# Optimization experiments

Measured on AMD Instinct MI355X. Metric: run time of the kernel, lower is better.

The kernel has to match this reference:

```python
import jax, jax.numpy as jnp
import numpy as np

EPS = 1e-7

def _sample_project(feat, pid, w1, b1, w2, b2):
    # feat: [B, C, H, W]; pid: [P] flat spatial indices into H*W
    B, C, H, W = feat.shape
    fr = jnp.transpose(feat, (0, 2, 3, 1)).reshape(B, H * W, C)  # [B, HW, C]
    x = fr[:, pid, :].reshape(B * pid.shape[0], C)               # gather -> [B*P, C]
    x = jnp.maximum(x @ w1 + b1, 0.0) @ w2 + b2                  # 2-layer MLP
    norm = jnp.sqrt(jnp.sum(x * x, axis=1, keepdims=True))       # L2 over channels
    return x / (norm + EPS)


def setup_inputs() -> dict:
    key = jax.random.key(0)
    ks = jax.random.split(key, 16)
    NC = 256
    shapes = [(16, 256, 128, 128), (16, 512, 64, 64), (16, 1024, 32, 32)]
    inp = {}
    for i, s in enumerate(shapes):
        inp[f"feat{i}"] = jax.random.normal(ks[i], s, dtype=jnp.float32)
        hw = s[2] * s[3]
        inp[f"patch_id{i}"] = jax.random.randint(ks[3 + i], (256,), 0, hw, dtype=jnp.int64)
        C = s[1]
        g = 0.02  # init_gain (normal init)
        inp[f"w1_{i}"] = g * jax.random.normal(ks[6 + 3 * i], (C, NC), dtype=jnp.float32)
        inp[f"b1_{i}"] = jnp.zeros((NC,), dtype=jnp.float32)
        inp[f"w2_{i}"] = g * jax.random.normal(ks[7 + 3 * i], (NC, NC), dtype=jnp.float32)
        inp[f"b2_{i}"] = jnp.zeros((NC,), dtype=jnp.float32)
    return inp


def reference(feat0, feat1, feat2, patch_id0, patch_id1, patch_id2,
              w1_0, b1_0, w2_0, b2_0,
              w1_1, b1_1, w2_1, b2_1,
              w1_2, b1_2, w2_2, b2_2):
    out0 = _sample_project(feat0, patch_id0, w1_0, b1_0, w2_0, b2_0)
    out1 = _sample_project(feat1, patch_id1, w1_1, b1_1, w2_1, b2_1)
    out2 = _sample_project(feat2, patch_id2, w1_2, b1_2, w2_2, b2_2)
    return (out0, out1, out2)
```

## Files before the change

kernel.cpp:

```cpp
#include <hip/hip_runtime.h>

typedef __attribute__((ext_vector_type(8))) short short8;
typedef __attribute__((ext_vector_type(4))) short short4v;
typedef __attribute__((ext_vector_type(4))) float floatx4;
typedef __attribute__((ext_vector_type(4))) unsigned int uintx4;

__device__ __forceinline__ short f2bf(float f) {
    unsigned u = __builtin_bit_cast(unsigned, f);
    u = (u + 0x7FFFu + ((u >> 16) & 1u)) >> 16;
    return (short)u;
}

#define W1T0 0
#define W1T1 65536
#define W1T2 196608
#define W2T0 458752
#define W2T1 524288
#define W2T2 589824
#define XG0  655360
#define XG1  1703936
#define XG2  3801088
#define LUT0 7995392
#define LUT1 8011776
#define LUT2 8015872

__global__ __launch_bounds__(256) void prep(
    const float* __restrict__ w10, const float* __restrict__ w11, const float* __restrict__ w12,
    const float* __restrict__ w20, const float* __restrict__ w21, const float* __restrict__ w22,
    const int* __restrict__ p0, const int* __restrict__ p1, const int* __restrict__ p2,
    unsigned short* __restrict__ wsb)
{
    int blk = blockIdx.x;
    int t = threadIdx.x;
    if (blk == 640) {
        short* lut = (short*)(wsb + LUT0);
        for (int i = t; i < 21504; i += 256) lut[i] = -1;
        __syncthreads();
        if (t < 256) {
            ((short*)(wsb + LUT0))[p0[t]] = (short)t;
            ((short*)(wsb + LUT1))[p1[t]] = (short)t;
            ((short*)(wsb + LUT2))[p2[t]] = (short)t;
        }
        return;
    }
    __shared__ float tile[32][33];
    const float* in; unsigned short* out; int K, t0;
    if (blk < 64)       { in = w10; out = wsb + W1T0; K = 256;  t0 = 0; }
    else if (blk < 192) { in = w11; out = wsb + W1T1; K = 512;  t0 = 64; }
    else if (blk < 448) { in = w12; out = wsb + W1T2; K = 1024; t0 = 192; }
    else if (blk < 512) { in = w20; out = wsb + W2T0; K = 256;  t0 = 448; }
    else if (blk < 576) { in = w21; out = wsb + W2T1; K = 256;  t0 = 512; }
    else                { in = w22; out = wsb + W2T2; K = 256;  t0 = 576; }
    int tile_id = blk - t0;
    int tk = K >> 5;
    int k0 = (tile_id % tk) << 5;
    int n0 = (tile_id / tk) << 5;
    int j = t & 31, i0 = (t >> 5) << 2;
    #pragma unroll
    for (int u = 0; u < 4; u++)
        tile[i0 + u][j] = in[(size_t)(k0 + i0 + u) * 256 + (n0 + j)];
    __syncthreads();
    int kf = t & 31, nf0 = (t >> 5) << 2;
    #pragma unroll
    for (int u = 0; u < 4; u++)
        out[(size_t)(n0 + nf0 + u) * K + (k0 + kf)] = (unsigned short)f2bf(tile[kf][nf0 + u]);
}

__global__ __launch_bounds__(256) void stage(
    const float* __restrict__ f0, const float* __restrict__ f1, const float* __restrict__ f2,
    const int* __restrict__ p0,
    unsigned short* __restrict__ wsb)
{
    __shared__ unsigned short tile[256 * 40];
    __shared__ int flags[256];
    int blk = blockIdx.x;
    int t = threadIdx.x;

    if (blk < 512) {
        int q = (blk << 8) + t;
        int row = q >> 5, c0 = (q & 31) << 3;
        int b = row >> 8, pp = row & 255;
        int s = p0[pp];
        const float* src = f0 + ((size_t)b * 256 + c0) * 16384 + s;
        float v[8];
        #pragma unroll
        for (int j = 0; j < 8; j++) v[j] = src[(size_t)j * 16384];
        short8 sv;
        #pragma unroll
        for (int j = 0; j < 8; j++) sv[j] = f2bf(v[j]);
        *(short8*)(wsb + XG0 + (size_t)row * 256 + c0) = sv;
        return;
    }

    const float* feat; const short* lut; unsigned short* xg;
    int C, HW, b, c0, hw0;
    if (blk < 1536) {
        int idx = blk - 512;
        feat = f1; lut = (const short*)(wsb + LUT1); xg = wsb + XG1;
        C = 512; HW = 4096;
        b = idx >> 6; int rem = idx & 63;
        c0 = (rem >> 2) << 5; hw0 = (rem & 3) << 10;
    } else {
        int idx = blk - 1536;
        feat = f2; lut = (const short*)(wsb + LUT2); xg = wsb + XG2;
        C = 1024; HW = 1024;
        b = idx >> 5; c0 = (idx & 31) << 5; hw0 = 0;
    }
    flags[t] = 0;
    __syncthreads();

    int cl = t >> 3, sub = t & 7;
    const float* fr = feat + ((size_t)b * C + c0 + cl) * HW + hw0;
    const short* lr = lut + hw0;
    for (int i = 0; i < 32; i++) {
        int hw = i * 32 + sub * 4;
        floatx4 v = *(const floatx4*)(fr + hw);
        short4v l4 = *(const short4v*)(lr + hw);
        #pragma unroll
        for (int j = 0; j < 4; j++) {
            int pv = l4[j];
            if (pv >= 0) {
                tile[pv * 40 + cl] = (unsigned short)f2bf(v[j]);
                flags[pv] = 1;
            }
        }
    }
    __syncthreads();
    if (flags[t]) {
        uintx4* d = (uintx4*)(xg + (size_t)(b * 256 + t) * C + c0);
        const uintx4* s4 = (const uintx4*)(tile + t * 40);
        d[0] = s4[0]; d[1] = s4[1]; d[2] = s4[2]; d[3] = s4[3];
    }
}

__global__ __launch_bounds__(256) void mlp(
    const float* __restrict__ b1_0, const float* __restrict__ b1_1, const float* __restrict__ b1_2,
    const float* __restrict__ b2_0, const float* __restrict__ b2_1, const float* __restrict__ b2_2,
    const int* __restrict__ p0, const int* __restrict__ p1, const int* __restrict__ p2,
    const unsigned short* __restrict__ wsb,
    float* __restrict__ out)
{
    __shared__ __align__(16) unsigned short hs[16 * 264];
    __shared__ float rs[16];

    int blk = blockIdx.x;
    int scale = 2 - (blk >> 8);
    int mblk = blk & 255;

    const float *b1, *b2; const int* pid;
    const unsigned short *w1T, *w2T, *xg; const short* lut;
    int C; size_t outBase;
    if (scale == 0)      { b1 = b1_0; b2 = b2_0; pid = p0; lut = (const short*)(wsb + LUT0);
                           w1T = wsb + W1T0; w2T = wsb + W2T0; xg = wsb + XG0; C = 256;  outBase = 0; }
    else if (scale == 1) { b1 = b1_1; b2 = b2_1; pid = p1; lut = (const short*)(wsb + LUT1);
                           w1T = wsb + W1T1; w2T = wsb + W2T1; xg = wsb + XG1; C = 512;  outBase = 1048576; }
    else                 { b1 = b1_2; b2 = b2_2; pid = p2; lut = (const short*)(wsb + LUT2);
                           w1T = wsb + W1T2; w2T = wsb + W2T2; xg = wsb + XG2; C = 1024; outBase = 2097152; }

    int t = threadIdx.x, wid = t >> 6, lane = t & 63, quad = lane >> 4, l15 = lane & 15;
    int c0 = wid << 6;
    int rowBase = mblk << 4;
    int myRow = rowBase + l15;
    int b = myRow >> 8, pp = myRow & 255;
    int w = lut[pid[pp]];
    const unsigned short* aBase = xg + (size_t)(b * 256 + w) * C;

    floatx4 acc[4];
    #pragma unroll
    for (int f = 0; f < 4; f++) acc[f] = (floatx4){0.f, 0.f, 0.f, 0.f};

    for (int kc = 0; kc < C; kc += 64) {
        short8 a0 = *(const short8*)(aBase + kc + quad * 8);
        short8 a1 = *(const short8*)(aBase + kc + 32 + quad * 8);
        #pragma unroll
        for (int f = 0; f < 4; f++) {
            const unsigned short* wr = w1T + (size_t)(c0 + f * 16 + l15) * C + kc;
            short8 bv0 = *(const short8*)(wr + quad * 8);
            short8 bv1 = *(const short8*)(wr + 32 + quad * 8);
            acc[f] = __builtin_amdgcn_mfma_f32_16x16x32_bf16(a0, bv0, acc[f], 0, 0, 0);
            acc[f] = __builtin_amdgcn_mfma_f32_16x16x32_bf16(a1, bv1, acc[f], 0, 0, 0);
        }
    }

    #pragma unroll
    for (int f = 0; f < 4; f++) {
        float bias = b1[c0 + f * 16 + l15];
        #pragma unroll
        for (int r = 0; r < 4; r++) {
            float h = fmaxf(acc[f][r] + bias, 0.f);
            hs[(quad * 4 + r) * 264 + (c0 + f * 16 + l15)] = (unsigned short)f2bf(h);
        }
    }
    if (t < 16) rs[t] = 0.f;
    __syncthreads();

    #pragma unroll
    for (int f = 0; f < 4; f++) acc[f] = (floatx4){0.f, 0.f, 0.f, 0.f};
    const unsigned short* hA = hs + l15 * 264;
    for (int kc = 0; kc < 256; kc += 64) {
        short8 a0 = *(const short8*)(hA + kc + quad * 8);
        short8 a1 = *(const short8*)(hA + kc + 32 + quad * 8);
        #pragma unroll
        for (int f = 0; f < 4; f++) {
            const unsigned short* wr = w2T + (size_t)(c0 + f * 16 + l15) * 256 + kc;
            short8 bv0 = *(const short8*)(wr + quad * 8);
            short8 bv1 = *(const short8*)(wr + 32 + quad * 8);
            acc[f] = __builtin_amdgcn_mfma_f32_16x16x32_bf16(a0, bv0, acc[f], 0, 0, 0);
            acc[f] = __builtin_amdgcn_mfma_f32_16x16x32_bf16(a1, bv1, acc[f], 0, 0, 0);
        }
    }

    float bias2[4];
    #pragma unroll
    for (int f = 0; f < 4; f++) bias2[f] = b2[c0 + f * 16 + l15];
    float psq[4] = {0.f, 0.f, 0.f, 0.f};
    #pragma unroll
    for (int f = 0; f < 4; f++)
        #pragma unroll
        for (int r = 0; r < 4; r++) {
            float yv = acc[f][r] + bias2[f];
            acc[f][r] = yv;
            psq[r] += yv * yv;
        }
    #pragma unroll
    for (int m = 1; m < 16; m <<= 1)
        #pragma unroll
        for (int r = 0; r < 4; r++)
            psq[r] += __shfl_xor(psq[r], m, 16);
    if (l15 == 0) {
        #pragma unroll
        for (int r = 0; r < 4; r++)
            atomicAdd(&rs[quad * 4 + r], psq[r]);
    }
    __syncthreads();

    #pragma unroll
    for (int f = 0; f < 4; f++)
        #pragma unroll
        for (int r = 0; r < 4; r++) {
            int row = quad * 4 + r;
            float inv = 1.f / (sqrtf(rs[row]) + 1e-7f);
            out[outBase + (size_t)(rowBase + row) * 256 + (c0 + f * 16 + l15)] =
                acc[f][r] * inv;
        }
}

extern "C" void kernel_launch(void* const* d_in, const int* in_sizes, int n_in,
                              void* d_out, int out_size, void* d_ws, size_t ws_size,
                              hipStream_t stream)
{
    (void)n_in; (void)out_size; (void)ws_size;
    bool dict = (in_sizes[1] == 256);
    const float *feat[3], *w1[3], *b1[3], *w2[3], *b2[3];
    const int* pid[3];
    for (int i = 0; i < 3; i++) {
        if (dict) {
            feat[i] = (const float*)d_in[i * 6 + 0];
            pid[i]  = (const int*)  d_in[i * 6 + 1];
            w1[i]   = (const float*)d_in[i * 6 + 2];
            b1[i]   = (const float*)d_in[i * 6 + 3];
            w2[i]   = (const float*)d_in[i * 6 + 4];
            b2[i]   = (const float*)d_in[i * 6 + 5];
        } else {
            feat[i] = (const float*)d_in[i];
            pid[i]  = (const int*)  d_in[3 + i];
            w1[i]   = (const float*)d_in[6 + 4 * i + 0];
            b1[i]   = (const float*)d_in[6 + 4 * i + 1];
            w2[i]   = (const float*)d_in[6 + 4 * i + 2];
            b2[i]   = (const float*)d_in[6 + 4 * i + 3];
        }
    }
    unsigned short* wsb = (unsigned short*)d_ws;
    prep<<<641, 256, 0, stream>>>(w1[0], w1[1], w1[2], w2[0], w2[1], w2[2],
                                  pid[0], pid[1], pid[2], wsb);
    stage<<<2048, 256, 0, stream>>>(feat[0], feat[1], feat[2], pid[0], wsb);
    mlp<<<768, 256, 0, stream>>>(b1[0], b1[1], b1[2],
                                 b2[0], b2[1], b2[2],
                                 pid[0], pid[1], pid[2],
                                 wsb, (float*)d_out);
}
```

Measured before the change: 548.4 us.

## Merge prep into stage, build per-block shared LUTs, retile MLP to 64 rows

Folds the weight transpose/convert work and global LUT construction into the stage kernel, removing one launch. Each staging block now builds its own patch-index LUT in shared memory, using atomicMax to resolve duplicate ids. Scale 0 now uses the same streaming scatter path as the other scales instead of a strided gather, so all of feat0 is read. The MLP kernel now processes 64 rows per block with a 4x4 MFMA fragment grid. This cuts the number of blocks and the repeated weight loads, but uses more registers and gives fewer blocks for parallelism.

After: 611.9 us. +11.6%, slower.

```diff
diff --git a/kernel.cpp b/kernel.cpp
--- a/kernel.cpp
+++ b/kernel.cpp
@@ -1,7 +1,7 @@
 #include <hip/hip_runtime.h>
 
 typedef __attribute__((ext_vector_type(8))) short short8;
-typedef __attribute__((ext_vector_type(4))) short short4v;
+typedef __attribute__((ext_vector_type(4))) int int4v;
 typedef __attribute__((ext_vector_type(4))) float floatx4;
 typedef __attribute__((ext_vector_type(4))) unsigned int uintx4;
 
@@ -20,102 +20,90 @@
 #define XG0  655360
 #define XG1  1703936
 #define XG2  3801088
-#define LUT0 7995392
-#define LUT1 8011776
-#define LUT2 8015872
-
-__global__ __launch_bounds__(256) void prep(
+#define LUTG 7995392
+
+__global__ __launch_bounds__(256) void stage(
+    const float* __restrict__ f0, const float* __restrict__ f1, const float* __restrict__ f2,
+    const int* __restrict__ p0, const int* __restrict__ p1, const int* __restrict__ p2,
     const float* __restrict__ w10, const float* __restrict__ w11, const float* __restrict__ w12,
     const float* __restrict__ w20, const float* __restrict__ w21, const float* __restrict__ w22,
-    const int* __restrict__ p0, const int* __restrict__ p1, const int* __restrict__ p2,
     unsigned short* __restrict__ wsb)
 {
+    __shared__ __align__(16) unsigned char smemraw[37888];
     int blk = blockIdx.x;
     int t = threadIdx.x;
-    if (blk == 640) {
-        short* lut = (short*)(wsb + LUT0);
-        for (int i = t; i < 21504; i += 256) lut[i] = -1;
+
+    if (blk >= 1280) {
+        if (blk == 1920) {
+            int* lutg = (int*)(wsb + LUTG);
+            for (int i = t; i < 21504; i += 256) lutg[i] = -1;
+            __syncthreads();
+            atomicMax(&lutg[p0[t]], t);
+            atomicMax(&lutg[16384 + p1[t]], t);
+            atomicMax(&lutg[20480 + p2[t]], t);
+            return;
+        }
+        float (*tileF)[33] = (float(*)[33])smemraw;
+        int b2 = blk - 1280;
+        const float* in; unsigned short* out; int K, t0;
+        if (b2 < 64)       { in = w10; out = wsb + W1T0; K = 256;  t0 = 0; }
+        else if (b2 < 192) { in = w11; out = wsb + W1T1; K = 512;  t0 = 64; }
+        else if (b2 < 448) { in = w12; out = wsb + W1T2; K = 1024; t0 = 192; }
+        else if (b2 < 512) { in = w20; out = wsb + W2T0; K = 256;  t0 = 448; }
+        else if (b2 < 576) { in = w21; out = wsb + W2T1; K = 256;  t0 = 512; }
+        else               { in = w22; out = wsb + W2T2; K = 256;  t0 = 576; }
+        int tile_id = b2 - t0;
+        int tk = K >> 5;
+        int k0 = (tile_id % tk) << 5;
+        int n0 = (tile_id / tk) << 5;
+        int j = t & 31, i0 = (t >> 5) << 2;
+        #pragma unroll
+        for (int u = 0; u < 4; u++)
+            tileF[i0 + u][j] = in[(size_t)(k0 + i0 + u) * 256 + (n0 + j)];
         __syncthreads();
-        if (t < 256) {
-            ((short*)(wsb + LUT0))[p0[t]] = (short)t;
-            ((short*)(wsb + LUT1))[p1[t]] = (short)t;
-            ((short*)(wsb + LUT2))[p2[t]] = (short)t;
-        }
+        int kf = t & 31, nf0 = (t >> 5) << 2;
+        #pragma unroll
+        for (int u = 0; u < 4; u++)
+            out[(size_t)(n0 + nf0 + u) * K + (k0 + kf)] = (unsigned short)f2bf(tileF[kf][nf0 + u]);
         return;
     }
-    __shared__ float tile[32][33];
-    const float* in; unsigned short* out; int K, t0;
-    if (blk < 64)       { in = w10; out = wsb + W1T0; K = 256;  t0 = 0; }
-    else if (blk < 192) { in = w11; out = wsb + W1T1; K = 512;  t0 = 64; }
-    else if (blk < 448) { in = w12; out = wsb + W1T2; K = 1024; t0 = 192; }
-    else if (blk < 512) { in = w20; out = wsb + W2T0; K = 256;  t0 = 448; }
-    else if (blk < 576) { in = w21; out = wsb + W2T1; K = 256;  t0 = 512; }
-    else                { in = w22; out = wsb + W2T2; K = 256;  t0 = 576; }
-    int tile_id = blk - t0;
-    int tk = K >> 5;
-    int k0 = (tile_id % tk) << 5;
-    int n0 = (tile_id / tk) << 5;
-    int j = t & 31, i0 = (t >> 5) << 2;
-    #pragma unroll
-    for (int u = 0; u < 4; u++)
-        tile[i0 + u][j] = in[(size_t)(k0 + i0 + u) * 256 + (n0 + j)];
-    __syncthreads();
-    int kf = t & 31, nf0 = (t >> 5) << 2;
-    #pragma unroll
-    for (int u = 0; u < 4; u++)
-        out[(size_t)(n0 + nf0 + u) * K + (k0 + kf)] = (unsigned short)f2bf(tile[kf][nf0 + u]);
-}
-
-__global__ __launch_bounds__(256) void stage(
-    const float* __restrict__ f0, const float* __restrict__ f1, const float* __restrict__ f2,
-    const int* __restrict__ p0,
-    unsigned short* __restrict__ wsb)
-{
-    __shared__ unsigned short tile[256 * 40];
-    __shared__ int flags[256];
-    int blk = blockIdx.x;
-    int t = threadIdx.x;
-
+
+    int* lut = (int*)smemraw;
+    unsigned short* tile = (unsigned short*)(smemraw + 16384);
+    int* flags = (int*)(smemraw + 16384 + 20480);
+
+    const float* feat; const int* pid; unsigned short* xg;
+    int C, HW, b, c0, hw0, seg;
     if (blk < 512) {
-        int q = (blk << 8) + t;
-        int row = q >> 5, c0 = (q & 31) << 3;
-        int b = row >> 8, pp = row & 255;
-        int s = p0[pp];
-        const float* src = f0 + ((size_t)b * 256 + c0) * 16384 + s;
-        float v[8];
-        #pragma unroll
-        for (int j = 0; j < 8; j++) v[j] = src[(size_t)j * 16384];
-        short8 sv;
-        #pragma unroll
-        for (int j = 0; j < 8; j++) sv[j] = f2bf(v[j]);
-        *(short8*)(wsb + XG0 + (size_t)row * 256 + c0) = sv;
-        return;
-    }
-
-    const float* feat; const short* lut; unsigned short* xg;
-    int C, HW, b, c0, hw0;
-    if (blk < 1536) {
+        feat = f0; pid = p0; xg = wsb + XG0; C = 256; HW = 16384;
+        b = blk >> 5; int rem = blk & 31;
+        c0 = (rem >> 2) << 5; hw0 = (rem & 3) << 12; seg = 4096;
+    } else if (blk < 768) {
         int idx = blk - 512;
-        feat = f1; lut = (const short*)(wsb + LUT1); xg = wsb + XG1;
-        C = 512; HW = 4096;
-        b = idx >> 6; int rem = idx & 63;
-        c0 = (rem >> 2) << 5; hw0 = (rem & 3) << 10;
+        feat = f1; pid = p1; xg = wsb + XG1; C = 512; HW = 4096;
+        b = idx >> 4; c0 = (idx & 15) << 5; hw0 = 0; seg = 4096;
     } else {
-        int idx = blk - 1536;
-        feat = f2; lut = (const short*)(wsb + LUT2); xg = wsb + XG2;
-        C = 1024; HW = 1024;
-        b = idx >> 5; c0 = (idx & 31) << 5; hw0 = 0;
-    }
+        int idx = blk - 768;
+        feat = f2; pid = p2; xg = wsb + XG2; C = 1024; HW = 1024;
+        b = idx >> 5; c0 = (idx & 31) << 5; hw0 = 0; seg = 1024;
+    }
+
+    for (int i = t; i < seg; i += 256) lut[i] = -1;
     flags[t] = 0;
+    __syncthreads();
+    {
+        int s = pid[t] - hw0;
+        if ((unsigned)s < (unsigned)seg) atomicMax(&lut[s], t);
+    }
     __syncthreads();
 
     int cl = t >> 3, sub = t & 7;
     const float* fr = feat + ((size_t)b * C + c0 + cl) * HW + hw0;
-    const short* lr = lut + hw0;
-    for (int i = 0; i < 32; i++) {
-        int hw = i * 32 + sub * 4;
+    int iters = seg >> 5;
+    for (int i = 0; i < iters; i++) {
+        int hw = (i << 5) + (sub << 2);
         floatx4 v = *(const floatx4*)(fr + hw);
-        short4v l4 = *(const short4v*)(lr + hw);
+        int4v l4 = *(const int4v*)(lut + hw);
         #pragma unroll
         for (int j = 0; j < 4; j++) {
             int pv = l4[j];
@@ -133,115 +121,135 @@
     }
 }
 
-__global__ __launch_bounds__(256) void mlp(
+__global__ __launch_bounds__(256, 2) void mlp(
     const float* __restrict__ b1_0, const float* __restrict__ b1_1, const float* __restrict__ b1_2,
     const float* __restrict__ b2_0, const float* __restrict__ b2_1, const float* __restrict__ b2_2,
     const int* __restrict__ p0, const int* __restrict__ p1, const int* __restrict__ p2,
     const unsigned short* __restrict__ wsb,
     float* __restrict__ out)
 {
-    __shared__ __align__(16) unsigned short hs[16 * 264];
-    __shared__ float rs[16];
+    __shared__ __align__(16) unsigned short hs[64 * 264];
+    __shared__ float rs[64];
 
     int blk = blockIdx.x;
-    int scale = 2 - (blk >> 8);
-    int mblk = blk & 255;
+    int scale = 2 - (blk >> 6);
+    int mblk = blk & 63;
 
     const float *b1, *b2; const int* pid;
-    const unsigned short *w1T, *w2T, *xg; const short* lut;
+    const unsigned short *w1T, *w2T, *xg; const int* lutg;
     int C; size_t outBase;
-    if (scale == 0)      { b1 = b1_0; b2 = b2_0; pid = p0; lut = (const short*)(wsb + LUT0);
+    const int* lutgB = (const int*)(wsb + LUTG);
+    if (scale == 0)      { b1 = b1_0; b2 = b2_0; pid = p0; lutg = lutgB;
                            w1T = wsb + W1T0; w2T = wsb + W2T0; xg = wsb + XG0; C = 256;  outBase = 0; }
-    else if (scale == 1) { b1 = b1_1; b2 = b2_1; pid = p1; lut = (const short*)(wsb + LUT1);
+    else if (scale == 1) { b1 = b1_1; b2 = b2_1; pid = p1; lutg = lutgB + 16384;
                            w1T = wsb + W1T1; w2T = wsb + W2T1; xg = wsb + XG1; C = 512;  outBase = 1048576; }
-    else                 { b1 = b1_2; b2 = b2_2; pid = p2; lut = (const short*)(wsb + LUT2);
+    else                 { b1 = b1_2; b2 = b2_2; pid = p2; lutg = lutgB + 20480;
                            w1T = wsb + W1T2; w2T = wsb + W2T2; xg = wsb + XG2; C = 1024; outBase = 2097152; }
 
     int t = threadIdx.x, wid = t >> 6, lane = t & 63, quad = lane >> 4, l15 = lane & 15;
     int c0 = wid << 6;
-    int rowBase = mblk << 4;
-    int myRow = rowBase + l15;
-    int b = myRow >> 8, pp = myRow & 255;
-    int w = lut[pid[pp]];
-    const unsigned short* aBase = xg + (size_t)(b * 256 + w) * C;
-
-    floatx4 acc[4];
-    #pragma unroll
-    for (int f = 0; f < 4; f++) acc[f] = (floatx4){0.f, 0.f, 0.f, 0.f};
-
-    for (int kc = 0; kc < C; kc += 64) {
-        short8 a0 = *(const short8*)(aBase + kc + quad * 8);
-        short8 a1 = *(const short8*)(aBase + kc + 32 + quad * 8);
-        #pragma unroll
-        for (int f = 0; f < 4; f++) {
-            const unsigned short* wr = w1T + (size_t)(c0 + f * 16 + l15) * C + kc;
-            short8 bv0 = *(const short8*)(wr + quad * 8);
-            short8 bv1 = *(const short8*)(wr + 32 + quad * 8);
-            acc[f] = __builtin_amdgcn_mfma_f32_16x16x32_bf16(a0, bv0, acc[f], 0, 0, 0);
-            acc[f] = __builtin_amdgcn_mfma_f32_16x16x32_bf16(a1, bv1, acc[f], 0, 0, 0);
-        }
-    }
-
-    #pragma unroll
-    for (int f = 0; f < 4; f++) {
-        float bias = b1[c0 + f * 16 + l15];
+    int rowBase = mblk << 6;
+
+    const unsigned short* aB[4];
+    #pragma unroll
+    for (int rf = 0; rf < 4; rf++) {
+        int row = rowBase + rf * 16 + l15;
+        int b = row >> 8, pp = row & 255;
+        int w = lutg[pid[pp]];
+        aB[rf] = xg + (size_t)(b * 256 + w) * C;
+    }
+
+    floatx4 acc[4][4];
+    #pragma unroll
+    for (int rf = 0; rf < 4; rf++)
+        #pragma unroll
+        for (int cf = 0; cf < 4; cf++) acc[rf][cf] = (floatx4){0.f, 0.f, 0.f, 0.f};
+
+    for (int kc = 0; kc < C; kc += 32) {
+        short8 a[4], bv[4];
+        #pragma unroll
+        for (int rf = 0; rf < 4; rf++)
+            a[rf] = *(const short8*)(aB[rf] + kc + quad * 8);
+        #pragma unroll
+        for (int cf = 0; cf < 4; cf++)
+            bv[cf] = *(const short8*)(w1T + (size_t)(c0 + cf * 16 + l15) * C + kc + quad * 8);
+        #pragma unroll
+        for (int rf = 0; rf < 4; rf++)
+            #pragma unroll
+            for (int cf = 0; cf < 4; cf++)
+                acc[rf][cf] = __builtin_amdgcn_mfma_f32_16x16x32_bf16(a[rf], bv[cf], acc[rf][cf], 0, 0, 0);
+    }
+
+    #pragma unroll
+    for (int cf = 0; cf < 4; cf++) {
+        float bias = b1[c0 + cf * 16 + l15];
+        #pragma unroll
+        for (int rf = 0; rf < 4; rf++)
+            #pragma unroll
+            for (int r = 0; r < 4; r++) {
+                float h = fmaxf(acc[rf][cf][r] + bias, 0.f);
+                hs[(rf * 16 + quad * 4 + r) * 264 + (c0 + cf * 16 + l15)] = (unsigned short)f2bf(h);
+            }
+    }
+    if (t < 64) rs[t] = 0.f;
+    __syncthreads();
+
+    #pragma unroll
+    for (int rf = 0; rf < 4; rf++)
+        #pragma unroll
+        for (int cf = 0; cf < 4; cf++) acc[rf][cf] = (floatx4){0.f, 0.f, 0.f, 0.f};
+    for (int kc = 0; kc < 256; kc += 32) {
+        short8 a[4], bv[4];
+        #pragma unroll
+        for (int rf = 0; rf < 4; rf++)
+            a[rf] = *(const short8*)(hs + (size_t)(rf * 16 + l15) * 264 + kc + quad * 8);
+        #pragma unroll
+        for (int cf = 0; cf < 4; cf++)
+            bv[cf] = *(const short8*)(w2T + (size_t)(c0 + cf * 16 + l15) * 256 + kc + quad * 8);
+        #pragma unroll
+        for (int rf = 0; rf < 4; rf++)
+            #pragma unroll
+            for (int cf = 0; cf < 4; cf++)
+                acc[rf][cf] = __builtin_amdgcn_mfma_f32_16x16x32_bf16(a[rf], bv[cf], acc[rf][cf], 0, 0, 0);
+    }
+
+    float bias2[4];
+    #pragma unroll
+    for (int cf = 0; cf < 4; cf++) bias2[cf] = b2[c0 + cf * 16 + l15];
+    #pragma unroll
+    for (int rf = 0; rf < 4; rf++) {
+        float psq[4] = {0.f, 0.f, 0.f, 0.f};
+        #pragma unroll
+        for (int cf = 0; cf < 4; cf++)
+            #pragma unroll
+            for (int r = 0; r < 4; r++) {
+                float yv = acc[rf][cf][r] + bias2[cf];
+                acc[rf][cf][r] = yv;
+                psq[r] += yv * yv;
+            }
+        #pragma unroll
+        for (int m = 1; m < 16; m <<= 1)
+            #pragma unroll
+            for (int r = 0; r < 4; r++)
+                psq[r] += __shfl_xor(psq[r], m, 16);
+        if (l15 == 0) {
+            #pragma unroll
+            for (int r = 0; r < 4; r++)
+                atomicAdd(&rs[rf * 16 + quad * 4 + r], psq[r]);
+        }
+    }
+    __syncthreads();
+
+    #pragma unroll
+    for (int rf = 0; rf < 4; rf++)
         #pragma unroll
         for (int r = 0; r < 4; r++) {
-            float h = fmaxf(acc[f][r] + bias, 0.f);
-            hs[(quad * 4 + r) * 264 + (c0 + f * 16 + l15)] = (unsigned short)f2bf(h);
-        }
-    }
-    if (t < 16) rs[t] = 0.f;
-    __syncthreads();
-
-    #pragma unroll
-    for (int f = 0; f < 4; f++) acc[f] = (floatx4){0.f, 0.f, 0.f, 0.f};
-    const unsigned short* hA = hs + l15 * 264;
-    for (int kc = 0; kc < 256; kc += 64) {
-        short8 a0 = *(const short8*)(hA + kc + quad * 8);
-        short8 a1 = *(const short8*)(hA + kc + 32 + quad * 8);
-        #pragma unroll
-        for (int f = 0; f < 4; f++) {
-            const unsigned short* wr = w2T + (size_t)(c0 + f * 16 + l15) * 256 + kc;
-            short8 bv0 = *(const short8*)(wr + quad * 8);
-            short8 bv1 = *(const short8*)(wr + 32 + quad * 8);
-            acc[f] = __builtin_amdgcn_mfma_f32_16x16x32_bf16(a0, bv0, acc[f], 0, 0, 0);
-            acc[f] = __builtin_amdgcn_mfma_f32_16x16x32_bf16(a1, bv1, acc[f], 0, 0, 0);
-        }
-    }
-
-    float bias2[4];
-    #pragma unroll
-    for (int f = 0; f < 4; f++) bias2[f] = b2[c0 + f * 16 + l15];
-    float psq[4] = {0.f, 0.f, 0.f, 0.f};
-    #pragma unroll
-    for (int f = 0; f < 4; f++)
-        #pragma unroll
-        for (int r = 0; r < 4; r++) {
-            float yv = acc[f][r] + bias2[f];
-            acc[f][r] = yv;
-            psq[r] += yv * yv;
-        }
-    #pragma unroll
-    for (int m = 1; m < 16; m <<= 1)
-        #pragma unroll
-        for (int r = 0; r < 4; r++)
-            psq[r] += __shfl_xor(psq[r], m, 16);
-    if (l15 == 0) {
-        #pragma unroll
-        for (int r = 0; r < 4; r++)
-            atomicAdd(&rs[quad * 4 + r], psq[r]);
-    }
-    __syncthreads();
-
-    #pragma unroll
-    for (int f = 0; f < 4; f++)
-        #pragma unroll
-        for (int r = 0; r < 4; r++) {
-            int row = quad * 4 + r;
+            int row = rf * 16 + quad * 4 + r;
             float inv = 1.f / (sqrtf(rs[row]) + 1e-7f);
-            out[outBase + (size_t)(rowBase + row) * 256 + (c0 + f * 16 + l15)] =
-                acc[f][r] * inv;
+            #pragma unroll
+            for (int cf = 0; cf < 4; cf++)
+                out[outBase + (size_t)(rowBase + row) * 256 + (c0 + cf * 16 + l15)] =
+                    acc[rf][cf][r] * inv;
         }
 }
 
@@ -271,10 +279,11 @@
         }
     }
     unsigned short* wsb = (unsigned short*)d_ws;
-    prep<<<641, 256, 0, stream>>>(w1[0], w1[1], w1[2], w2[0], w2[1], w2[2],
-                                  pid[0], pid[1], pid[2], wsb);
-    stage<<<2048, 256, 0, stream>>>(feat[0], feat[1], feat[2], pid[0], wsb);
-    mlp<<<768, 256, 0, stream>>>(b1[0], b1[1], b1[2],
+    stage<<<1921, 256, 0, stream>>>(feat[0], feat[1], feat[2],
+                                    pid[0], pid[1], pid[2],
+                                    w1[0], w1[1], w1[2],
+                                    w2[0], w2[1], w2[2], wsb);
+    mlp<<<192, 256, 0, stream>>>(b1[0], b1[1], b1[2],
                                  b2[0], b2[1], b2[2],
                                  pid[0], pid[1], pid[2],
                                  wsb, (float*)d_out);
```
